# Kernel tuning notes

Measured on AMD Instinct MI355X. Metric: run time of the kernel, lower is better.

## Reference

```python
import jax, jax.numpy as jnp
import numpy as np

OUTPUT_SIZE = (48, 48, 48)
TRUNCATION = (32, 32, 32)
HOMOMORPHIC = False


def dct_mat(N):
    """Orthonormal DCT-II matrix M so that y = M @ x matches scipy dct(x, norm='ortho')."""
    n = jnp.arange(N, dtype=jnp.float32)
    k = n[:, None]
    M = jnp.cos(jnp.pi * (n[None, :] + 0.5) * k / N) * jnp.sqrt(2.0 / N)
    M = M.at[0].mul(1.0 / jnp.sqrt(2.0))  # k=0 row scale -> sqrt(1/N)
    return M


def setup_inputs() -> dict:
    key = jax.random.key(0)
    x = jax.random.normal(key, (4, 32, 64, 64, 64), dtype=jnp.float32)
    return {"x": x}


def reference(x) -> jnp.ndarray:
    B, C, D, H, W = x.shape
    t0, t1, t2 = TRUNCATION
    o0, o1, o2 = OUTPUT_SIZE

    if HOMOMORPHIC:
        x = jnp.log(x + 1e-6)

    # 3D orthonormal DCT-II (separable, per axis)
    Md, Mh, Mw = dct_mat(D), dct_mat(H), dct_mat(W)
    xd = jnp.einsum('ad,bcdhw->bcahw', Md, x)
    xd = jnp.einsum('ah,bcdhw->bcdaw', Mh, xd)
    xd = jnp.einsum('aw,bcdhw->bcdha', Mw, xd)

    # crop low frequencies, zero-pad to output_size
    xc = xd[:, :, :t0, :t1, :t2]
    xp = jnp.pad(xc, ((0, 0), (0, 0), (0, o0 - t0), (0, o1 - t1), (0, o2 - t2)))

    # 3D orthonormal IDCT (DCT-III) = transpose of DCT-II matrix
    Id, Ih, Iw = dct_mat(o0).T, dct_mat(o1).T, dct_mat(o2).T
    y = jnp.einsum('ad,bcdhw->bcahw', Id, xp)
    y = jnp.einsum('ah,bcdhw->bcdaw', Ih, y)
    y = jnp.einsum('aw,bcdhw->bcdha', Iw, y)

    if HOMOMORPHIC:
        y = jnp.exp(y)
    return y
```

## Files before the change

### kernel.cpp

```cpp
#include <hip/hip_runtime.h>


typedef __attribute__((ext_vector_type(8))) short short8;
typedef __attribute__((ext_vector_type(4))) float f32x4;
typedef __attribute__((ext_vector_type(4))) unsigned int u32x4;
typedef __attribute__((ext_vector_type(2))) unsigned int u32x2;

static __device__ __forceinline__ unsigned short f2bf(float f) {
    unsigned int u = __float_as_uint(f);
    u += 0x7fffu + ((u >> 16) & 1u);
    return (unsigned short)(u >> 16);
}
static __device__ __forceinline__ float bf2f(unsigned short h) {
    return __uint_as_float(((unsigned int)h) << 16);
}

static __device__ __forceinline__ short8 ldtbl(const unsigned short* __restrict__ tbl,
                                               int s, int ks, int t, int l) {
    return *(const short8*)(tbl + (unsigned)((((s * 2 + ks) * 3 + t) * 64 + l) * 8));
}

__global__ __launch_bounds__(256) void gen_tbl(unsigned short* __restrict__ tbl) {
    int i = blockIdx.x * 256 + threadIdx.x;
    int j = i & 7;
    int lane = (i >> 3) & 63;
    int tks = i >> 9;
    int t = tks % 3, ks = tks / 3;
    int k = 8 * (lane >> 4) + j + 32 * ks;
    int a = 16 * t + (lane & 15);
    const float PI = 3.14159265358979323846f;
    const float s48 = 0.20412414523193150818f;
    const float s64 = 0.17677669529663688110f;
    float s = 0.f;
    for (int kk = 0; kk < 32; ++kk) {
        int m48 = ((2 * a + 1) * kk) % 192;
        int m64 = ((2 * k + 1) * kk) % 256;
        float c48 = cosf(PI * (float)m48 / 96.0f) * s48;
        float c64 = cosf(PI * (float)m64 / 128.0f) * s64;
        if (kk == 0) { c48 *= 0.70710678118654752440f; c64 *= 0.70710678118654752440f; }
        s += c48 * c64;
    }
    unsigned short hi = f2bf(s);
    unsigned short lo = f2bf(s - bf2f(hi));
    tbl[i] = hi;
    tbl[i + 3072] = lo;
}

#define SC_S 72
__global__ __launch_bounds__(256) void k1_wh(const float* __restrict__ x,
                                             const unsigned short* __restrict__ tbl,
                                             unsigned short* __restrict__ y2) {
    __shared__ unsigned short sC[48 * SC_S];

    const int tid = threadIdx.x;
    const int blk = blockIdx.x;
    const int g = __builtin_amdgcn_readfirstlane(tid >> 6);
    const int l = tid & 63;
    const int r = l & 15;
    const int kq = l >> 4;

    f32x4 z = {0.f, 0.f, 0.f, 0.f};
    f32x4 acc0 = z, acc1 = z, acc2 = z;
    const float* xb = x + (unsigned)(blk * 4096 + (16 * g + r) * 64 + kq * 8);
    #pragma unroll
    for (int ks = 0; ks < 2; ++ks) {
        float4 xa = *(const float4*)(xb + 32 * ks);
        float4 xc = *(const float4*)(xb + 32 * ks + 4);
        float v[8] = {xa.x, xa.y, xa.z, xa.w, xc.x, xc.y, xc.z, xc.w};
        short8 xh, xl;
        #pragma unroll
        for (int j = 0; j < 8; ++j) {
            unsigned int u = __float_as_uint(v[j]);
            float rem = v[j] - __uint_as_float(u & 0xffff0000u);
            xh[j] = (short)(u >> 16);
            xl[j] = (short)(__float_as_uint(rem) >> 16);
        }
        #pragma unroll
        for (int t = 0; t < 3; ++t) {
            short8 wh = ldtbl(tbl, 0, ks, t, l);
            f32x4 a = (t == 0) ? acc0 : (t == 1) ? acc1 : acc2;
            a = __builtin_amdgcn_mfma_f32_16x16x32_bf16(xh, wh, a, 0, 0, 0);
            a = __builtin_amdgcn_mfma_f32_16x16x32_bf16(xl, wh, a, 0, 0, 0);
            if (t == 0) acc0 = a; else if (t == 1) acc1 = a; else acc2 = a;
        }
    }
    #pragma unroll
    for (int t = 0; t < 3; ++t) {
        f32x4 a = (t == 0) ? acc0 : (t == 1) ? acc1 : acc2;
        u32x2 pk;
        pk[0] = (unsigned int)f2bf(a[0]) | ((unsigned int)f2bf(a[1]) << 16);
        pk[1] = (unsigned int)f2bf(a[2]) | ((unsigned int)f2bf(a[3]) << 16);
        *(u32x2*)&sC[(16 * t + r) * SC_S + 16 * g + 4 * kq] = pk;
    }
    __syncthreads();

    auto loadA = [&](int m, int ks) -> short8 {
        return *(const short8*)&sC[(16 * m + r) * SC_S + 8 * kq + 32 * ks];
    };
    auto storeY = [&](int m, int n, f32x4 c) {
        u32x2 pk;
        pk[0] = (unsigned int)f2bf(c[0]) | ((unsigned int)f2bf(c[1]) << 16);
        pk[1] = (unsigned int)f2bf(c[2]) | ((unsigned int)f2bf(c[3]) << 16);
        *(u32x2*)(y2 + (unsigned)(blk * 2304 + (16 * n + r) * 48 + 16 * m + 4 * kq)) = pk;
    };

    if (g < 3) {
        f32x4 c0 = z, c1 = z;
        #pragma unroll
        for (int ks = 0; ks < 2; ++ks) {
            short8 ah = ldtbl(tbl, 0, ks, g, l);
            c0 = __builtin_amdgcn_mfma_f32_16x16x32_bf16(loadA(0, ks), ah, c0, 0, 0, 0);
            c1 = __builtin_amdgcn_mfma_f32_16x16x32_bf16(loadA(1, ks), ah, c1, 0, 0, 0);
        }
        storeY(0, g, c0);
        storeY(1, g, c1);
    } else {
        f32x4 t0 = z, t1 = z, t2 = z;
        #pragma unroll
        for (int ks = 0; ks < 2; ++ks) {
            short8 ca = loadA(2, ks);
            t0 = __builtin_amdgcn_mfma_f32_16x16x32_bf16(ca, ldtbl(tbl, 0, ks, 0, l), t0, 0, 0, 0);
            t1 = __builtin_amdgcn_mfma_f32_16x16x32_bf16(ca, ldtbl(tbl, 0, ks, 1, l), t1, 0, 0, 0);
            t2 = __builtin_amdgcn_mfma_f32_16x16x32_bf16(ca, ldtbl(tbl, 0, ks, 2, l), t2, 0, 0, 0);
        }
        storeY(2, 0, t0);
        storeY(2, 1, t1);
        storeY(2, 2, t2);
    }
}

__global__ __launch_bounds__(256) void k2_d(const unsigned short* __restrict__ y2,
                                            const unsigned short* __restrict__ tbl,
                                            float* __restrict__ out) {
    __shared__ unsigned short sY[4 * 3 * 64 * 16];

    const int tid = threadIdx.x;
    const int blk = blockIdx.x;
    const int bc = blk / 12;
    const int quad = blk % 12;

    const unsigned short* yb = y2 + (unsigned)(bc * 64 * 2304 + quad * 4 * 48);
    #pragma unroll
    for (int jj = 0; jj < 6; ++jj) {
        int f = tid + 256 * jj;
        int d = f / 24;
        int p = f % 24;
        int a1l = p / 6;
        int q = p % 6;
        int a2 = q * 8;
        int m = a2 >> 4;
        int c0 = a2 & 15;
        u32x4 v = *(const u32x4*)(yb + (unsigned)(d * 2304 + a1l * 48 + a2));
        *(u32x4*)&sY[(((a1l * 3 + m) * 64) + d) * 16 + c0] = v;
    }
    __syncthreads();

    const int g = __builtin_amdgcn_readfirstlane(tid >> 6);
    const int l = tid & 63;
    const int r = l & 15;
    const int kq = l >> 4;
    const int a1 = quad * 4 + g;

    short8 th[2][3], tl[2][3];
    #pragma unroll
    for (int ks = 0; ks < 2; ++ks)
        #pragma unroll
        for (int n = 0; n < 3; ++n) {
            th[ks][n] = ldtbl(tbl, 0, ks, n, l);
            tl[ks][n] = ldtbl(tbl, 1, ks, n, l);
        }

    f32x4 z = {0.f, 0.f, 0.f, 0.f};
    f32x4 acc[3][3];
    #pragma unroll
    for (int m = 0; m < 3; ++m)
        #pragma unroll
        for (int n = 0; n < 3; ++n) acc[m][n] = z;

    #pragma unroll
    for (int m = 0; m < 3; ++m) {
        #pragma unroll
        for (int ks = 0; ks < 2; ++ks) {
            short8 ya;
            #pragma unroll
            for (int j = 0; j < 8; ++j)
                ya[j] = (short)sY[((g * 3 + m) * 64 + 8 * kq + 32 * ks + j) * 16 + r];
            #pragma unroll
            for (int n = 0; n < 3; ++n) {
                acc[m][n] = __builtin_amdgcn_mfma_f32_16x16x32_bf16(ya, th[ks][n], acc[m][n], 0, 0, 0);
                acc[m][n] = __builtin_amdgcn_mfma_f32_16x16x32_bf16(ya, tl[ks][n], acc[m][n], 0, 0, 0);
            }
        }
    }

    #pragma unroll
    for (int m = 0; m < 3; ++m)
        #pragma unroll
        for (int n = 0; n < 3; ++n) {
            float4 v;
            v.x = acc[m][n][0]; v.y = acc[m][n][1]; v.z = acc[m][n][2]; v.w = acc[m][n][3];
            float* dst = out + ((size_t)(bc * 48 + 16 * n + r) * 48 + a1) * 48 + 16 * m + 4 * kq;
            *(float4*)dst = v;
        }
}

extern "C" void kernel_launch(void* const* d_in, const int* in_sizes, int n_in,
                              void* d_out, int out_size, void* d_ws, size_t ws_size,
                              hipStream_t stream) {
    const float* x = (const float*)d_in[0];
    float* out = (float*)d_out;

    unsigned short* tbl = (unsigned short*)d_ws;
    unsigned short* y2 = (unsigned short*)((char*)d_ws + 65536);

    gen_tbl<<<12, 256, 0, stream>>>(tbl);
    k1_wh<<<128 * 64, 256, 0, stream>>>(x, tbl, y2);
    k2_d<<<128 * 12, 256, 0, stream>>>(y2, tbl, out);
}
```

Measured before the change: 61.59 us.

## Restructure intermediate layout so D-pass reads contiguous fragments without LDS staging

The first kernel now loops over 8 depth slices per block, packs the bf16 results of consecutive depths into registers, and writes an intermediate laid out with depth innermost in groups of 8. The second kernel can then load its MFMA A-fragments straight from global memory, which drops the LDS staging, the strided 16-bit LDS gathers and a barrier. Block indices are remapped so that the blocks handling one batch-channel are grouped by XCD, and input loads and output stores use nontemporal hints. The cost is fewer and larger blocks in the first kernel, more barriers inside its depth loop, and higher register pressure from the packed output buffer.

```diff
diff --git a/kernel.cpp b/kernel.cpp
--- a/kernel.cpp
+++ b/kernel.cpp
@@ -35,8 +35,8 @@
     for (int kk = 0; kk < 32; ++kk) {
         int m48 = ((2 * a + 1) * kk) % 192;
         int m64 = ((2 * k + 1) * kk) % 256;
-        float c48 = cosf(PI * (float)m48 / 96.0f) * s48;
-        float c64 = cosf(PI * (float)m64 / 128.0f) * s64;
+        float c48 = __cosf(PI * (float)m48 / 96.0f) * s48;
+        float c64 = __cosf(PI * (float)m64 / 128.0f) * s64;
         if (kk == 0) { c48 *= 0.70710678118654752440f; c64 *= 0.70710678118654752440f; }
         s += c48 * c64;
     }
@@ -46,6 +46,7 @@
     tbl[i + 3072] = lo;
 }
 
+
 #define SC_S 72
 __global__ __launch_bounds__(256) void k1_wh(const float* __restrict__ x,
                                              const unsigned short* __restrict__ tbl,
@@ -54,113 +55,125 @@
 
     const int tid = threadIdx.x;
     const int blk = blockIdx.x;
+    const int xcd = blk & 7;
+    const int rest = blk >> 3;
+    const int bc = xcd * 16 + (rest & 15);
+    const int dg = rest >> 4;
     const int g = __builtin_amdgcn_readfirstlane(tid >> 6);
     const int l = tid & 63;
     const int r = l & 15;
     const int kq = l >> 4;
 
+    u32x4 ob[3][4];
     f32x4 z = {0.f, 0.f, 0.f, 0.f};
-    f32x4 acc0 = z, acc1 = z, acc2 = z;
-    const float* xb = x + (unsigned)(blk * 4096 + (16 * g + r) * 64 + kq * 8);
-    #pragma unroll
-    for (int ks = 0; ks < 2; ++ks) {
-        float4 xa = *(const float4*)(xb + 32 * ks);
-        float4 xc = *(const float4*)(xb + 32 * ks + 4);
-        float v[8] = {xa.x, xa.y, xa.z, xa.w, xc.x, xc.y, xc.z, xc.w};
-        short8 xh, xl;
-        #pragma unroll
-        for (int j = 0; j < 8; ++j) {
-            unsigned int u = __float_as_uint(v[j]);
-            float rem = v[j] - __uint_as_float(u & 0xffff0000u);
-            xh[j] = (short)(u >> 16);
-            xl[j] = (short)(__float_as_uint(rem) >> 16);
+
+    #pragma unroll
+    for (int dd = 0; dd < 8; ++dd) {
+        f32x4 acc0 = z, acc1 = z, acc2 = z;
+        const float* xb = x + (unsigned)((bc * 64 + dg * 8 + dd) * 4096
+                                         + (16 * g + r) * 64 + kq * 8);
+        #pragma unroll
+        for (int ks = 0; ks < 2; ++ks) {
+            f32x4 xa = __builtin_nontemporal_load((const f32x4*)(xb + 32 * ks));
+            f32x4 xc = __builtin_nontemporal_load((const f32x4*)(xb + 32 * ks + 4));
+            float v[8] = {xa[0], xa[1], xa[2], xa[3], xc[0], xc[1], xc[2], xc[3]};
+            short8 xh, xl;
+            #pragma unroll
+            for (int j = 0; j < 8; ++j) {
+                unsigned int u = __float_as_uint(v[j]);
+                float rem = v[j] - __uint_as_float(u & 0xffff0000u);
+                xh[j] = (short)(u >> 16);
+                xl[j] = (short)(__float_as_uint(rem) >> 16);
+            }
+            #pragma unroll
+            for (int t = 0; t < 3; ++t) {
+                short8 wh = ldtbl(tbl, 0, ks, t, l);
+                f32x4 a = (t == 0) ? acc0 : (t == 1) ? acc1 : acc2;
+                a = __builtin_amdgcn_mfma_f32_16x16x32_bf16(xh, wh, a, 0, 0, 0);
+                a = __builtin_amdgcn_mfma_f32_16x16x32_bf16(xl, wh, a, 0, 0, 0);
+                if (t == 0) acc0 = a; else if (t == 1) acc1 = a; else acc2 = a;
+            }
         }
         #pragma unroll
         for (int t = 0; t < 3; ++t) {
-            short8 wh = ldtbl(tbl, 0, ks, t, l);
             f32x4 a = (t == 0) ? acc0 : (t == 1) ? acc1 : acc2;
-            a = __builtin_amdgcn_mfma_f32_16x16x32_bf16(xh, wh, a, 0, 0, 0);
-            a = __builtin_amdgcn_mfma_f32_16x16x32_bf16(xl, wh, a, 0, 0, 0);
-            if (t == 0) acc0 = a; else if (t == 1) acc1 = a; else acc2 = a;
-        }
+            u32x2 pk;
+            pk[0] = (unsigned int)f2bf(a[0]) | ((unsigned int)f2bf(a[1]) << 16);
+            pk[1] = (unsigned int)f2bf(a[2]) | ((unsigned int)f2bf(a[3]) << 16);
+            *(u32x2*)&sC[(16 * t + r) * SC_S + 16 * g + 4 * kq] = pk;
+        }
+        __syncthreads();
+
+        #define LOADA(m, ks) (*(const short8*)&sC[(16 * (m) + r) * SC_S + 8 * kq + 32 * (ks)])
+        if (g < 3) {
+            f32x4 c0 = z, c1 = z;
+            #pragma unroll
+            for (int ks = 0; ks < 2; ++ks) {
+                short8 ah = ldtbl(tbl, 0, ks, g, l);
+                c0 = __builtin_amdgcn_mfma_f32_16x16x32_bf16(LOADA(0, ks), ah, c0, 0, 0, 0);
+                c1 = __builtin_amdgcn_mfma_f32_16x16x32_bf16(LOADA(1, ks), ah, c1, 0, 0, 0);
+            }
+            #pragma unroll
+            for (int rr = 0; rr < 4; ++rr) {
+                unsigned int b0 = f2bf(c0[rr]), b1 = f2bf(c1[rr]);
+                if ((dd & 1) == 0) { ob[0][rr][dd >> 1] = b0;  ob[1][rr][dd >> 1] = b1; }
+                else { ob[0][rr][dd >> 1] |= b0 << 16;  ob[1][rr][dd >> 1] |= b1 << 16; }
+            }
+        } else {
+            f32x4 t0 = z, t1 = z, t2 = z;
+            #pragma unroll
+            for (int ks = 0; ks < 2; ++ks) {
+                short8 ca = LOADA(2, ks);
+                t0 = __builtin_amdgcn_mfma_f32_16x16x32_bf16(ca, ldtbl(tbl, 0, ks, 0, l), t0, 0, 0, 0);
+                t1 = __builtin_amdgcn_mfma_f32_16x16x32_bf16(ca, ldtbl(tbl, 0, ks, 1, l), t1, 0, 0, 0);
+                t2 = __builtin_amdgcn_mfma_f32_16x16x32_bf16(ca, ldtbl(tbl, 0, ks, 2, l), t2, 0, 0, 0);
+            }
+            #pragma unroll
+            for (int rr = 0; rr < 4; ++rr) {
+                unsigned int b0 = f2bf(t0[rr]), b1 = f2bf(t1[rr]), b2 = f2bf(t2[rr]);
+                if ((dd & 1) == 0) {
+                    ob[0][rr][dd >> 1] = b0; ob[1][rr][dd >> 1] = b1; ob[2][rr][dd >> 1] = b2;
+                } else {
+                    ob[0][rr][dd >> 1] |= b0 << 16; ob[1][rr][dd >> 1] |= b1 << 16; ob[2][rr][dd >> 1] |= b2 << 16;
+                }
+            }
+        }
+        __syncthreads();
     }
-    #pragma unroll
-    for (int t = 0; t < 3; ++t) {
-        f32x4 a = (t == 0) ? acc0 : (t == 1) ? acc1 : acc2;
-        u32x2 pk;
-        pk[0] = (unsigned int)f2bf(a[0]) | ((unsigned int)f2bf(a[1]) << 16);
-        pk[1] = (unsigned int)f2bf(a[2]) | ((unsigned int)f2bf(a[3]) << 16);
-        *(u32x2*)&sC[(16 * t + r) * SC_S + 16 * g + 4 * kq] = pk;
-    }
-    __syncthreads();
-
-    auto loadA = [&](int m, int ks) -> short8 {
-        return *(const short8*)&sC[(16 * m + r) * SC_S + 8 * kq + 32 * ks];
-    };
-    auto storeY = [&](int m, int n, f32x4 c) {
-        u32x2 pk;
-        pk[0] = (unsigned int)f2bf(c[0]) | ((unsigned int)f2bf(c[1]) << 16);
-        pk[1] = (unsigned int)f2bf(c[2]) | ((unsigned int)f2bf(c[3]) << 16);
-        *(u32x2*)(y2 + (unsigned)(blk * 2304 + (16 * n + r) * 48 + 16 * m + 4 * kq)) = pk;
-    };
-
+
+    unsigned short* yo = y2 + (unsigned)(bc * 147456 + dg * 18432);
     if (g < 3) {
-        f32x4 c0 = z, c1 = z;
-        #pragma unroll
-        for (int ks = 0; ks < 2; ++ks) {
-            short8 ah = ldtbl(tbl, 0, ks, g, l);
-            c0 = __builtin_amdgcn_mfma_f32_16x16x32_bf16(loadA(0, ks), ah, c0, 0, 0, 0);
-            c1 = __builtin_amdgcn_mfma_f32_16x16x32_bf16(loadA(1, ks), ah, c1, 0, 0, 0);
-        }
-        storeY(0, g, c0);
-        storeY(1, g, c1);
+        #pragma unroll
+        for (int t = 0; t < 2; ++t)
+            #pragma unroll
+            for (int rr = 0; rr < 4; ++rr)
+                *(u32x4*)(yo + (unsigned)((16 * g + r) * 384 + (16 * t + 4 * kq + rr) * 8)) = ob[t][rr];
     } else {
-        f32x4 t0 = z, t1 = z, t2 = z;
-        #pragma unroll
-        for (int ks = 0; ks < 2; ++ks) {
-            short8 ca = loadA(2, ks);
-            t0 = __builtin_amdgcn_mfma_f32_16x16x32_bf16(ca, ldtbl(tbl, 0, ks, 0, l), t0, 0, 0, 0);
-            t1 = __builtin_amdgcn_mfma_f32_16x16x32_bf16(ca, ldtbl(tbl, 0, ks, 1, l), t1, 0, 0, 0);
-            t2 = __builtin_amdgcn_mfma_f32_16x16x32_bf16(ca, ldtbl(tbl, 0, ks, 2, l), t2, 0, 0, 0);
-        }
-        storeY(2, 0, t0);
-        storeY(2, 1, t1);
-        storeY(2, 2, t2);
+        #pragma unroll
+        for (int t = 0; t < 3; ++t)
+            #pragma unroll
+            for (int rr = 0; rr < 4; ++rr)
+                *(u32x4*)(yo + (unsigned)((16 * t + r) * 384 + (32 + 4 * kq + rr) * 8)) = ob[t][rr];
     }
 }
 
 __global__ __launch_bounds__(256) void k2_d(const unsigned short* __restrict__ y2,
                                             const unsigned short* __restrict__ tbl,
                                             float* __restrict__ out) {
-    __shared__ unsigned short sY[4 * 3 * 64 * 16];
-
     const int tid = threadIdx.x;
     const int blk = blockIdx.x;
-    const int bc = blk / 12;
-    const int quad = blk % 12;
-
-    const unsigned short* yb = y2 + (unsigned)(bc * 64 * 2304 + quad * 4 * 48);
-    #pragma unroll
-    for (int jj = 0; jj < 6; ++jj) {
-        int f = tid + 256 * jj;
-        int d = f / 24;
-        int p = f % 24;
-        int a1l = p / 6;
-        int q = p % 6;
-        int a2 = q * 8;
-        int m = a2 >> 4;
-        int c0 = a2 & 15;
-        u32x4 v = *(const u32x4*)(yb + (unsigned)(d * 2304 + a1l * 48 + a2));
-        *(u32x4*)&sY[(((a1l * 3 + m) * 64) + d) * 16 + c0] = v;
-    }
-    __syncthreads();
-
+    const int xcd = blk & 7;
+    const int rest = blk >> 3;
+    const int bc = xcd * 16 + rest / 12;
+    const int quad = rest % 12;
     const int g = __builtin_amdgcn_readfirstlane(tid >> 6);
     const int l = tid & 63;
     const int r = l & 15;
     const int kq = l >> 4;
     const int a1 = quad * 4 + g;
 
+    const unsigned short* yb = y2 + (unsigned)(bc * 147456 + a1 * 384);
+
     short8 th[2][3], tl[2][3];
     #pragma unroll
     for (int ks = 0; ks < 2; ++ks)
@@ -178,29 +191,24 @@
         for (int n = 0; n < 3; ++n) acc[m][n] = z;
 
     #pragma unroll
-    for (int m = 0; m < 3; ++m) {
+    for (int m = 0; m < 3; ++m)
         #pragma unroll
         for (int ks = 0; ks < 2; ++ks) {
-            short8 ya;
-            #pragma unroll
-            for (int j = 0; j < 8; ++j)
-                ya[j] = (short)sY[((g * 3 + m) * 64 + 8 * kq + 32 * ks + j) * 16 + r];
+            short8 ya = *(const short8*)(yb + (unsigned)((kq + 4 * ks) * 18432 + (16 * m + r) * 8));
             #pragma unroll
             for (int n = 0; n < 3; ++n) {
                 acc[m][n] = __builtin_amdgcn_mfma_f32_16x16x32_bf16(ya, th[ks][n], acc[m][n], 0, 0, 0);
                 acc[m][n] = __builtin_amdgcn_mfma_f32_16x16x32_bf16(ya, tl[ks][n], acc[m][n], 0, 0, 0);
             }
         }
-    }
 
     #pragma unroll
     for (int m = 0; m < 3; ++m)
         #pragma unroll
         for (int n = 0; n < 3; ++n) {
-            float4 v;
-            v.x = acc[m][n][0]; v.y = acc[m][n][1]; v.z = acc[m][n][2]; v.w = acc[m][n][3];
+            f32x4 v = acc[m][n];
             float* dst = out + ((size_t)(bc * 48 + 16 * n + r) * 48 + a1) * 48 + 16 * m + 4 * kq;
-            *(float4*)dst = v;
+            __builtin_nontemporal_store(v, (f32x4*)dst);
         }
 }
 
@@ -214,6 +222,6 @@
     unsigned short* y2 = (unsigned short*)((char*)d_ws + 65536);
 
     gen_tbl<<<12, 256, 0, stream>>>(tbl);
-    k1_wh<<<128 * 64, 256, 0, stream>>>(x, tbl, y2);
+    k1_wh<<<128 * 8, 256, 0, stream>>>(x, tbl, y2);
     k2_d<<<128 * 12, 256, 0, stream>>>(y2, tbl, out);
 }
```

After: 89.21 us. +44.9%, slower.
